# Performance work log

Hardware: AMD Instinct MI355X
Metric: run time of the kernel (lower is better)

Reference implementation:

```python
import jax, jax.numpy as jnp
import numpy as np

B, C, H, W = 2, 256, 128, 128
NUM_CLASSES = 80
HIDDEN = 4
STRIDE = 8
NMS_CAND = 1000
IOU_THR = 0.65
MAX_DET = 100
PRIOR_BIAS = float(-np.log((1.0 - 0.01) / 0.01))  # RetinaNet-style prior prob bias


def _conv1x1(x, w, b):
    # x: [B,C,H,W], w: [O,C], b: [O]
    return jnp.einsum('bchw,oc->bohw', x, w) + b[None, :, None, None]


def _head(x, w_in, b_in, w_hid, b_hid, w_out, b_out):
    # ProjConv in-layer -> residual ProjConv hidden layers (kernel_size=1, skip=True) -> ProjConv out-layer
    x = _conv1x1(x, w_in, b_in)
    def step(h, wb):
        w, b = wb
        return h + _conv1x1(h, w, b), None
    x, _ = jax.lax.scan(step, x, (w_hid, b_hid))
    return _conv1x1(x, w_out, b_out)


def _nms_keep(boxes):
    # boxes: [K,4] in xyxy, pre-sorted by descending score
    x1, y1, x2, y2 = boxes[:, 0], boxes[:, 1], boxes[:, 2], boxes[:, 3]
    area = jnp.clip(x2 - x1, 0) * jnp.clip(y2 - y1, 0)
    lt = jnp.maximum(boxes[:, None, :2], boxes[None, :, :2])
    rb = jnp.minimum(boxes[:, None, 2:], boxes[None, :, 2:])
    wh = jnp.clip(rb - lt, 0)
    inter = wh[..., 0] * wh[..., 1]
    iou = inter / (area[:, None] + area[None, :] - inter + 1e-6)
    idx = jnp.arange(NMS_CAND)
    def body(i, keep):
        sup = (iou[i] > IOU_THR) & (idx > i) & keep[i]
        return keep & ~sup
    return jax.lax.fori_loop(0, NMS_CAND, body, jnp.ones((NMS_CAND,), bool))


def setup_inputs() -> dict:
    key = jax.random.key(0)
    ks = jax.random.split(key, 10)
    s = 0.02
    d = {'feat': jax.random.normal(ks[0], (B, C, H, W), jnp.float32)}
    d['cls_w_in'] = s * jax.random.normal(ks[1], (C, C), jnp.float32)
    d['cls_b_in'] = jnp.zeros((C,), jnp.float32)
    d['cls_w_hid'] = s * jax.random.normal(ks[2], (HIDDEN, C, C), jnp.float32)
    d['cls_b_hid'] = jnp.zeros((HIDDEN, C), jnp.float32)
    d['cls_w_out'] = s * jax.random.normal(ks[3], (NUM_CLASSES + 1, C), jnp.float32)
    d['cls_b_out'] = jnp.full((NUM_CLASSES + 1,), PRIOR_BIAS, jnp.float32)
    d['obj_w_in'] = s * jax.random.normal(ks[4], (C, C), jnp.float32)
    d['obj_b_in'] = jnp.zeros((C,), jnp.float32)
    d['obj_w_hid'] = s * jax.random.normal(ks[5], (HIDDEN, C, C), jnp.float32)
    d['obj_b_hid'] = jnp.zeros((HIDDEN, C), jnp.float32)
    d['obj_w_out'] = s * jax.random.normal(ks[6], (2, C), jnp.float32)
    d['obj_b_out'] = jnp.full((2,), PRIOR_BIAS, jnp.float32)
    d['box_w_in'] = s * jax.random.normal(ks[7], (C, C), jnp.float32)
    d['box_b_in'] = jnp.zeros((C,), jnp.float32)
    d['box_w_hid'] = s * jax.random.normal(ks[8], (HIDDEN, C, C), jnp.float32)
    d['box_b_hid'] = jnp.zeros((HIDDEN, C), jnp.float32)
    d['box_w_out'] = s * jax.random.normal(ks[9], (4, C), jnp.float32)
    d['box_b_out'] = jnp.zeros((4,), jnp.float32)
    return d


def reference(feat, cls_w_in, cls_b_in, cls_w_hid, cls_b_hid, cls_w_out, cls_b_out,
              obj_w_in, obj_b_in, obj_w_hid, obj_b_hid, obj_w_out, obj_b_out,
              box_w_in, box_b_in, box_w_hid, box_b_hid, box_w_out, box_b_out):
    cls_logits = _head(feat, cls_w_in, cls_b_in, cls_w_hid, cls_b_hid, cls_w_out, cls_b_out)
    obj_logits = _head(feat, obj_w_in, obj_b_in, obj_w_hid, obj_b_hid, obj_w_out, obj_b_out)
    box_logits = _head(feat, box_w_in, box_b_in, box_w_hid, box_b_hid, box_w_out, box_b_out)

    # per-location scores: class prob (excluding background channel) * objectness prob
    cls_prob = jax.nn.sigmoid(cls_logits[:, :NUM_CLASSES])        # [B,80,H,W]
    obj_prob = jax.nn.sigmoid(obj_logits[:, :1])                  # [B,1,H,W]
    sc = cls_prob * obj_prob
    score = sc.max(axis=1).reshape(B, -1)                         # [B,HW]
    label = sc.argmax(axis=1).reshape(B, -1)                      # [B,HW]

    # FCOS-style decode of (l,t,r,b) deltas around grid points
    xs = (jnp.arange(W, dtype=feat.dtype) + 0.5) * STRIDE
    ys = (jnp.arange(H, dtype=feat.dtype) + 0.5) * STRIDE
    px = jnp.broadcast_to(xs[None, :], (H, W)).reshape(-1)
    py = jnp.broadcast_to(ys[:, None], (H, W)).reshape(-1)
    ltrb = jnp.exp(box_logits).reshape(B, 4, -1) * STRIDE         # [B,4,HW]
    boxes = jnp.stack([px[None] - ltrb[:, 0], py[None] - ltrb[:, 1],
                       px[None] + ltrb[:, 2], py[None] + ltrb[:, 3]], axis=-1)  # [B,HW,4]

    # candidate selection + NMS + final top detections
    cand_sc, idx = jax.lax.top_k(score, NMS_CAND)                 # sorted descending
    cand_box = jnp.take_along_axis(boxes, idx[:, :, None], axis=1)
    cand_lab = jnp.take_along_axis(label, idx, axis=1)
    keep = jax.vmap(_nms_keep)(cand_box)                          # [B,K] bool
    det_sc, fin_idx = jax.lax.top_k(cand_sc * keep, MAX_DET)
    det_box = jnp.take_along_axis(cand_box, fin_idx[:, :, None], axis=1)
    det_lab = jnp.take_along_axis(cand_lab, fin_idx, axis=1)
    return det_box, det_sc, det_lab
```

## Files before the change

### kernel.cpp

```cpp
#include <hip/hip_runtime.h>
#include <math.h>

typedef unsigned int u32;
typedef unsigned long long u64;

#define HWSZ 16384
#define NCAND 1000
#define CAP 1024
#define NDET 100

__device__ __forceinline__ float sigmoidf_(float x) {
  return 1.0f / (1.0f + expf(-x));
}

__device__ __forceinline__ void wave_stagger(int wid) {
  switch (wid) {
    case 1: __builtin_amdgcn_s_sleep(1); break;
    case 2: __builtin_amdgcn_s_sleep(2); break;
    case 3: __builtin_amdgcn_s_sleep(3); break;
    case 4: __builtin_amdgcn_s_sleep(4); break;
    case 5: __builtin_amdgcn_s_sleep(5); break;
    case 6: __builtin_amdgcn_s_sleep(6); break;
    case 7: __builtin_amdgcn_s_sleep(7); break;
    case 8: __builtin_amdgcn_s_sleep(8); break;
    case 9: __builtin_amdgcn_s_sleep(9); break;
    case 10: __builtin_amdgcn_s_sleep(10); break;
    case 11: __builtin_amdgcn_s_sleep(11); break;
    case 12: __builtin_amdgcn_s_sleep(12); break;
    case 13: __builtin_amdgcn_s_sleep(13); break;
    case 14: __builtin_amdgcn_s_sleep(14); break;
    case 15: __builtin_amdgcn_s_sleep(15); break;
    default: break;
  }
}

template <int NROWS, bool FULLROWS>
__device__ __forceinline__ void run_gemm(const float* __restrict__ Wm,
                                         const float (*X)[128], int rbase,
                                         int p0, float2 acc[16]) {
#pragma unroll
  for (int r = 0; r < 16; ++r) {
    acc[r].x = 0.f;
    acc[r].y = 0.f;
  }
  wave_stagger(rbase >> 4);
  if (rbase < NROWS) {
    for (int kb = 0; kb < 64; ++kb) {
      float2 xv0 = *(const float2*)&X[kb * 4 + 0][p0];
      float2 xv1 = *(const float2*)&X[kb * 4 + 1][p0];
      float2 xv2 = *(const float2*)&X[kb * 4 + 2][p0];
      float2 xv3 = *(const float2*)&X[kb * 4 + 3][p0];
#pragma unroll
      for (int r = 0; r < 16; ++r) {
        if (FULLROWS || rbase + r < NROWS) {
          const float4 wv =
              *(const float4*)(Wm + (size_t)(rbase + r) * 256 + kb * 4);
          acc[r].x += wv.x * xv0.x;
          acc[r].y += wv.x * xv0.y;
          acc[r].x += wv.y * xv1.x;
          acc[r].y += wv.y * xv1.y;
          acc[r].x += wv.z * xv2.x;
          acc[r].y += wv.z * xv2.y;
          acc[r].x += wv.w * xv3.x;
          acc[r].y += wv.w * xv3.y;
        }
      }
    }
  }
}

__global__ __launch_bounds__(1024, 4) void heads_fused(
    const float* __restrict__ feat, const float* __restrict__ ow_in,
    const float* __restrict__ ob_in, const float* __restrict__ ow_hid,
    const float* __restrict__ ob_hid, const float* __restrict__ ow_out,
    const float* __restrict__ ob_out, const float* __restrict__ cw_in,
    const float* __restrict__ cb_in, const float* __restrict__ cw_hid,
    const float* __restrict__ cb_hid, const float* __restrict__ cw_out,
    const float* __restrict__ cb_out, float* __restrict__ score,
    int* __restrict__ label) {
  __shared__ __align__(16) float X[256][128];
  __shared__ float objL[128];
  __shared__ float smax[5][128];
  __shared__ int sarg[5][128];

  const int tid = threadIdx.x;
  const int wid = __builtin_amdgcn_readfirstlane(tid >> 6);
  const int ln = tid & 63;
  const int p0 = 2 * ln;
  const int rbase = wid * 16;
  const int batch = blockIdx.x >> 7;
  const int pbase = (blockIdx.x & 127) * 128;
  const float* fb = feat + (size_t)batch * 256 * HWSZ;

  for (int head = 0; head < 2; ++head) {
    const float* w_in = head ? cw_in : ow_in;
    const float* b_in = head ? cb_in : ob_in;
    const float* w_hid = head ? cw_hid : ow_hid;
    const float* b_hid = head ? cb_hid : ob_hid;

#pragma unroll
    for (int m = 0; m < 8; ++m) {
      int f4 = tid + 1024 * m;
      int c = f4 >> 5, col4 = (f4 & 31) * 4;
      *(float4*)&X[c][col4] =
          *(const float4*)(fb + (size_t)c * HWSZ + pbase + col4);
    }
    __syncthreads();

    float2 acc[16];
    for (int s = 0; s < 5; ++s) {
      const float* Wm = (s == 0) ? w_in : (w_hid + (size_t)(s - 1) * 65536);
      const float* bs = (s == 0) ? b_in : (b_hid + (s - 1) * 256);
      run_gemm<256, true>(Wm, X, rbase, p0, acc);
      __syncthreads();
#pragma unroll
      for (int r = 0; r < 16; ++r) {
        float b = bs[rbase + r];
        float2 v = make_float2(acc[r].x + b, acc[r].y + b);
        if (s > 0) {
          v.x += X[rbase + r][p0];
          v.y += X[rbase + r][p0 + 1];
        }
        *(float2*)&X[rbase + r][p0] = v;
      }
      __syncthreads();
    }

    if (head == 0) {
      run_gemm<2, false>(ow_out, X, rbase, p0, acc);
      if (wid == 0) {
        float bo = ob_out[0];
        objL[p0] = sigmoidf_(acc[0].x + bo);
        objL[p0 + 1] = sigmoidf_(acc[0].y + bo);
      }
      __syncthreads();
    } else {
      run_gemm<80, true>(cw_out, X, rbase, p0, acc);
      if (rbase < 80) {
        float ob0 = objL[p0], ob1 = objL[p0 + 1];
        float best0 = -1.f, best1 = -1.f;
        int a0 = 0, a1 = 0;
#pragma unroll
        for (int r = 0; r < 16; ++r) {
          float bb = cb_out[rbase + r];
          float s0 = sigmoidf_(acc[r].x + bb) * ob0;
          float s1 = sigmoidf_(acc[r].y + bb) * ob1;
          if (s0 > best0) {
            best0 = s0;
            a0 = rbase + r;
          }
          if (s1 > best1) {
            best1 = s1;
            a1 = rbase + r;
          }
        }
        smax[wid][p0] = best0;
        sarg[wid][p0] = a0;
        smax[wid][p0 + 1] = best1;
        sarg[wid][p0 + 1] = a1;
      }
      __syncthreads();
      if (tid < 128) {
        float best = -1.f;
        int ba = 0;
        for (int g = 0; g < 5; ++g) {
          float m = smax[g][tid];
          if (m > best) {
            best = m;
            ba = sarg[g][tid];
          }
        }
        score[batch * HWSZ + pbase + tid] = best;
        label[batch * HWSZ + pbase + tid] = ba;
      }
    }
  }
}

__global__ __launch_bounds__(1024) void box_all(
    const float* __restrict__ feat, const int* __restrict__ cand_idx,
    const float* __restrict__ w_in, const float* __restrict__ b_in,
    const float* __restrict__ w_hid, const float* __restrict__ b_hid,
    const float* __restrict__ w_out, const float* __restrict__ b_out,
    float* __restrict__ cand_box) {
  __shared__ float h[256][8];
  const int tid = threadIdx.x;
  const int batch = blockIdx.x >> 7;
  const int cbase = (blockIdx.x & 127) * 8;
  const float* fb = feat + (size_t)batch * 256 * HWSZ;

  for (int i = tid; i < 2048; i += 1024) {
    int k = i >> 3, c = i & 7;
    int r = cbase + c;
    float v = 0.f;
    if (r < NCAND) {
      int hw = cand_idx[batch * CAP + r];
      v = fb[(size_t)k * HWSZ + hw];
    }
    h[k][c] = v;
  }
  __syncthreads();

  const int wid = tid >> 6, ln = tid & 63;
  const int c = ln & 7, rr = ln >> 3;
  const int r0 = wid * 16 + rr, r1 = wid * 16 + 8 + rr;

  for (int s = 0; s < 5; ++s) {
    const float* Wm = (s == 0) ? w_in : (w_hid + (size_t)(s - 1) * 65536);
    const float* bs = (s == 0) ? b_in : (b_hid + (s - 1) * 256);
    float a0 = 0.f, a1 = 0.f;
    for (int kb = 0; kb < 64; ++kb) {
      float4 w0 = *(const float4*)&Wm[(size_t)r0 * 256 + kb * 4];
      float4 w1 = *(const float4*)&Wm[(size_t)r1 * 256 + kb * 4];
      float x0 = h[kb * 4 + 0][c], x1 = h[kb * 4 + 1][c];
      float x2 = h[kb * 4 + 2][c], x3 = h[kb * 4 + 3][c];
      a0 += w0.x * x0;
      a0 += w0.y * x1;
      a0 += w0.z * x2;
      a0 += w0.w * x3;
      a1 += w1.x * x0;
      a1 += w1.y * x1;
      a1 += w1.z * x2;
      a1 += w1.w * x3;
    }
    __syncthreads();
    float v0 = a0 + bs[r0], v1 = a1 + bs[r1];
    if (s > 0) {
      v0 += h[r0][c];
      v1 += h[r1][c];
    }
    h[r0][c] = v0;
    h[r1][c] = v1;
    __syncthreads();
  }

  if (tid < 32) {
    int row = tid >> 3, cc = tid & 7;
    int r = cbase + cc;
    if (r < NCAND) {
      float s = 0.f;
      for (int k = 0; k < 256; ++k) s += w_out[row * 256 + k] * h[k][cc];
      s += b_out[row];
      float e = expf(s) * 8.f;
      int hw = cand_idx[batch * CAP + r];
      int hh = hw >> 7, wwp = hw & 127;
      float px = (wwp + 0.5f) * 8.f, py = (hh + 0.5f) * 8.f;
      float coord = (row == 0)   ? px - e
                    : (row == 1) ? py - e
                    : (row == 2) ? px + e
                                 : py + e;
      cand_box[(size_t)(batch * CAP + r) * 4 + row] = coord;
    }
  }
}

__device__ __forceinline__ void suffix2048(u32* hist, int tid) {
  for (int d = 1; d < 2048; d <<= 1) {
    u32 v0 = hist[tid] + ((tid + d < 2048) ? hist[tid + d] : 0u);
    u32 v1 =
        hist[tid + 1024] + ((tid + 1024 + d < 2048) ? hist[tid + 1024 + d] : 0u);
    __syncthreads();
    hist[tid] = v0;
    hist[tid + 1024] = v1;
    __syncthreads();
  }
}

__global__ __launch_bounds__(1024) void topk_kernel(
    const float* __restrict__ score, const int* __restrict__ label,
    float* __restrict__ cand_sc, int* __restrict__ cand_idx,
    int* __restrict__ cand_lab) {
  __shared__ u32 hist[2048];
  __shared__ u64 buf[CAP];
  __shared__ u32 tiebuf[2048];
  __shared__ int sres[2];
  __shared__ int cA, cT;
  const int tid = threadIdx.x;
  const int b = blockIdx.x;
  const int base = b * HWSZ;
  u32 bits[16];
#pragma unroll
  for (int m = 0; m < 16; ++m)
    bits[m] = __float_as_uint(score[base + tid + 1024 * m]);

  int K = NCAND;
  u32 hi = 0;
  u32 thresh = 0;
  for (int lev = 0; lev < 3; ++lev) {
    hist[tid] = 0;
    hist[tid + 1024] = 0;
    __syncthreads();
#pragma unroll
    for (int m = 0; m < 16; ++m) {
      u32 v = bits[m];
      bool ok;
      int bin;
      if (lev == 0) {
        ok = true;
        bin = v >> 21;
      } else if (lev == 1) {
        ok = ((v >> 21) == hi);
        bin = (v >> 10) & 2047;
      } else {
        ok = ((v >> 10) == hi);
        bin = v & 1023;
      }
      if (ok) atomicAdd(&hist[bin], 1u);
    }
    __syncthreads();
    suffix2048(hist, tid);
#pragma unroll
    for (int e = 0; e < 2; ++e) {
      int i = tid + e * 1024;
      int Si = (int)hist[i];
      int Sn = (i + 1 < 2048) ? (int)hist[i + 1] : 0;
      if (Si >= K && Sn < K) {
        sres[0] = i;
        sres[1] = Sn;
      }
    }
    __syncthreads();
    int B = sres[0];
    K -= sres[1];
    if (lev == 0) hi = (u32)B;
    else if (lev == 1) hi = (hi << 11) | (u32)B;
    else thresh = (hi << 10) | (u32)B;
    __syncthreads();
  }
  const int T = K;

  if (tid == 0) {
    cA = 0;
    cT = 0;
  }
  __syncthreads();
#pragma unroll
  for (int m = 0; m < 16; ++m) {
    u32 v = bits[m];
    int idxp = tid + 1024 * m;
    if (v > thresh) {
      int pos = atomicAdd(&cA, 1);
      buf[pos] = ((u64)(~v) << 32) | (u32)idxp;
    } else if (v == thresh) {
      int pos = atomicAdd(&cT, 1);
      if (pos < 2048) tiebuf[pos] = (u32)idxp;
    }
  }
  __syncthreads();
  const int A = cA;
  int nT = cT < 2048 ? cT : 2048;
  for (int i = tid; i < 2048; i += 1024)
    if (i >= nT) tiebuf[i] = 0xFFFFFFFFu;
  __syncthreads();
  if (nT > 1) {
    for (int k = 2; k <= 2048; k <<= 1)
      for (int j = k >> 1; j > 0; j >>= 1) {
#pragma unroll
        for (int e = 0; e < 2; ++e) {
          int i = tid + e * 1024;
          int l = i ^ j;
          if (l > i) {
            u32 a = tiebuf[i], bb = tiebuf[l];
            bool up = ((i & k) == 0);
            if ((a > bb) == up) {
              tiebuf[i] = bb;
              tiebuf[l] = a;
            }
          }
        }
        __syncthreads();
      }
  }
  for (int t2 = tid; t2 < T; t2 += 1024)
    buf[A + t2] = ((u64)(~thresh) << 32) | tiebuf[t2];
  for (int i = tid; i < CAP; i += 1024)
    if (i >= NCAND) buf[i] = 0xFFFFFFFFFFFFFFFFull;
  __syncthreads();
  for (int k = 2; k <= 1024; k <<= 1)
    for (int j = k >> 1; j > 0; j >>= 1) {
      int i = tid, l = i ^ j;
      if (l > i) {
        u64 a = buf[i], bb = buf[l];
        bool up = ((i & k) == 0);
        if ((a > bb) == up) {
          buf[i] = bb;
          buf[l] = a;
        }
      }
      __syncthreads();
    }
  if (tid < NCAND) {
    u64 kv = buf[tid];
    u32 sb = ~(u32)(kv >> 32);
    int pix = (int)(kv & 0xFFFFFFFFull);
    cand_sc[b * CAP + tid] = __uint_as_float(sb);
    cand_idx[b * CAP + tid] = pix;
    cand_lab[b * CAP + tid] = label[base + pix];
  }
}

__global__ __launch_bounds__(1024) void nms_mask(
    const float* __restrict__ cand_box, u64* __restrict__ mask) {
  int bid = blockIdx.x;
  int b = bid / NCAND, i = bid % NCAND;
  int j = threadIdx.x;
  const float* bi = cand_box + (size_t)(b * CAP + i) * 4;
  float ix1 = bi[0], iy1 = bi[1], ix2 = bi[2], iy2 = bi[3];
  bool pred = false;
  if (j < NCAND && j > i) {
    const float* bj = cand_box + (size_t)(b * CAP + j) * 4;
    float jx1 = bj[0], jy1 = bj[1], jx2 = bj[2], jy2 = bj[3];
    float ai = fmaxf(ix2 - ix1, 0.f) * fmaxf(iy2 - iy1, 0.f);
    float aj = fmaxf(jx2 - jx1, 0.f) * fmaxf(jy2 - jy1, 0.f);
    float lx = fmaxf(ix1, jx1), ly = fmaxf(iy1, jy1);
    float rx = fminf(ix2, jx2), ry = fminf(iy2, jy2);
    float w = fmaxf(rx - lx, 0.f), h = fmaxf(ry - ly, 0.f);
    float inter = w * h;
    float iou = inter / (ai + aj - inter + 1e-6f);
    pred = iou > 0.65f;
  }
  u64 word = __ballot(pred);
  if ((j & 63) == 0) mask[(size_t)b * 16384 + i * 16 + (j >> 6)] = word;
}

__global__ void nms_finish(const u64* __restrict__ mask,
                           const float* __restrict__ cand_sc,
                           const int* __restrict__ cand_lab,
                           const float* __restrict__ cand_box,
                           float* __restrict__ out) {
  __shared__ u64 M[16000];
  int b = blockIdx.x, lane = threadIdx.x;
  for (int m = lane; m < 16000; m += 64) M[m] = mask[(size_t)b * 16384 + m];
  __syncthreads();
  u64 kw = 0ull;
  if (lane < 15) kw = ~0ull;
  else if (lane == 15) kw = (1ull << 40) - 1;
  for (int i = 0; i < NCAND; ++i) {
    u64 wi = __shfl(kw, i >> 6);
    if ((wi >> (i & 63)) & 1ull) {
      if (lane < 16) kw &= ~M[i * 16 + lane];
    }
  }
  u64 valid = 0ull;
  if (lane < 15) valid = ~0ull;
  else if (lane == 15) valid = (1ull << 40) - 1;
  kw &= valid;
  u64 sup = valid & ~kw;
  int ck = __popcll(kw), cs = __popcll(sup);
  int preK = 0, preS = 0, totK = 0;
  for (int q = 0; q < 16; ++q) {
    int vk = __shfl(ck, q), vs = __shfl(cs, q);
    if (q < lane) {
      preK += vk;
      preS += vs;
    }
    totK += vk;
  }
  float* obox = out;
  float* osc = out + 2 * NDET * 4;
  float* olab = out + 2 * NDET * 4 + 2 * NDET;
  if (lane < 16) {
    u64 m = kw;
    int pos = preK;
    while (m) {
      int bit = __ffsll((unsigned long long)m) - 1;
      m &= m - 1;
      int j = lane * 64 + bit;
      if (pos < NDET) {
        osc[b * NDET + pos] = cand_sc[b * CAP + j];
        olab[b * NDET + pos] = (float)cand_lab[b * CAP + j];
        const float* bx = cand_box + (size_t)(b * CAP + j) * 4;
        float* dst = obox + (size_t)(b * NDET + pos) * 4;
        dst[0] = bx[0];
        dst[1] = bx[1];
        dst[2] = bx[2];
        dst[3] = bx[3];
      }
      ++pos;
    }
    m = sup;
    pos = totK + preS;
    while (m) {
      int bit = __ffsll((unsigned long long)m) - 1;
      m &= m - 1;
      int j = lane * 64 + bit;
      if (pos < NDET) {
        osc[b * NDET + pos] = 0.0f;
        olab[b * NDET + pos] = (float)cand_lab[b * CAP + j];
        const float* bx = cand_box + (size_t)(b * CAP + j) * 4;
        float* dst = obox + (size_t)(b * NDET + pos) * 4;
        dst[0] = bx[0];
        dst[1] = bx[1];
        dst[2] = bx[2];
        dst[3] = bx[3];
      }
      ++pos;
    }
  }
}

extern "C" void kernel_launch(void* const* d_in, const int* in_sizes, int n_in,
                              void* d_out, int out_size, void* d_ws,
                              size_t ws_size, hipStream_t stream) {
  (void)in_sizes;
  (void)n_in;
  (void)out_size;
  (void)ws_size;
  const float* feat = (const float*)d_in[0];
  const float* cls_w_in = (const float*)d_in[1];
  const float* cls_b_in = (const float*)d_in[2];
  const float* cls_w_hid = (const float*)d_in[3];
  const float* cls_b_hid = (const float*)d_in[4];
  const float* cls_w_out = (const float*)d_in[5];
  const float* cls_b_out = (const float*)d_in[6];
  const float* obj_w_in = (const float*)d_in[7];
  const float* obj_b_in = (const float*)d_in[8];
  const float* obj_w_hid = (const float*)d_in[9];
  const float* obj_b_hid = (const float*)d_in[10];
  const float* obj_w_out = (const float*)d_in[11];
  const float* obj_b_out = (const float*)d_in[12];
  const float* box_w_in = (const float*)d_in[13];
  const float* box_b_in = (const float*)d_in[14];
  const float* box_w_hid = (const float*)d_in[15];
  const float* box_b_hid = (const float*)d_in[16];
  const float* box_w_out = (const float*)d_in[17];
  const float* box_b_out = (const float*)d_in[18];
  float* out = (float*)d_out;

  char* w = (char*)d_ws;
  float* scoreArr = (float*)w;
  int* labelArr = (int*)(w + 131072);
  float* cand_sc = (float*)(w + 262144);
  int* cand_idx = (int*)(w + 270336);
  int* cand_lab = (int*)(w + 278528);
  float* cand_box = (float*)(w + 286720);
  u64* maskArr = (u64*)(w + 319488);

  heads_fused<<<256, 1024, 0, stream>>>(
      feat, obj_w_in, obj_b_in, obj_w_hid, obj_b_hid, obj_w_out, obj_b_out,
      cls_w_in, cls_b_in, cls_w_hid, cls_b_hid, cls_w_out, cls_b_out, scoreArr,
      labelArr);
  topk_kernel<<<2, 1024, 0, stream>>>(scoreArr, labelArr, cand_sc, cand_idx,
                                      cand_lab);
  box_all<<<256, 1024, 0, stream>>>(feat, cand_idx, box_w_in, box_b_in,
                                    box_w_hid, box_b_hid, box_w_out, box_b_out,
                                    cand_box);
  nms_mask<<<2000, 1024, 0, stream>>>(cand_box, maskArr);
  nms_finish<<<2, 64, 0, stream>>>(maskArr, cand_sc, cand_lab, cand_box, out);
}
```

Measured before the change: 783.3 us.

## Stage conv weights through double-buffered LDS instead of per-wave global loads

New measurement: 943.7 us. 1.2x slower.

```diff
diff --git a/kernel.cpp b/kernel.cpp
--- a/kernel.cpp
+++ b/kernel.cpp
@@ -13,59 +13,64 @@
   return 1.0f / (1.0f + expf(-x));
 }
 
-__device__ __forceinline__ void wave_stagger(int wid) {
-  switch (wid) {
-    case 1: __builtin_amdgcn_s_sleep(1); break;
-    case 2: __builtin_amdgcn_s_sleep(2); break;
-    case 3: __builtin_amdgcn_s_sleep(3); break;
-    case 4: __builtin_amdgcn_s_sleep(4); break;
-    case 5: __builtin_amdgcn_s_sleep(5); break;
-    case 6: __builtin_amdgcn_s_sleep(6); break;
-    case 7: __builtin_amdgcn_s_sleep(7); break;
-    case 8: __builtin_amdgcn_s_sleep(8); break;
-    case 9: __builtin_amdgcn_s_sleep(9); break;
-    case 10: __builtin_amdgcn_s_sleep(10); break;
-    case 11: __builtin_amdgcn_s_sleep(11); break;
-    case 12: __builtin_amdgcn_s_sleep(12); break;
-    case 13: __builtin_amdgcn_s_sleep(13); break;
-    case 14: __builtin_amdgcn_s_sleep(14); break;
-    case 15: __builtin_amdgcn_s_sleep(15); break;
-    default: break;
-  }
-}
-
 template <int NROWS, bool FULLROWS>
-__device__ __forceinline__ void run_gemm(const float* __restrict__ Wm,
-                                         const float (*X)[128], int rbase,
+__device__ __forceinline__ void gemm_lds(const float* __restrict__ Wm,
+                                         const float (*X)[128],
+                                         float (*Wb)[2048], int tid, int rbase,
                                          int p0, float2 acc[16]) {
 #pragma unroll
   for (int r = 0; r < 16; ++r) {
     acc[r].x = 0.f;
     acc[r].y = 0.f;
   }
-  wave_stagger(rbase >> 4);
-  if (rbase < NROWS) {
-    for (int kb = 0; kb < 64; ++kb) {
-      float2 xv0 = *(const float2*)&X[kb * 4 + 0][p0];
-      float2 xv1 = *(const float2*)&X[kb * 4 + 1][p0];
-      float2 xv2 = *(const float2*)&X[kb * 4 + 2][p0];
-      float2 xv3 = *(const float2*)&X[kb * 4 + 3][p0];
+  const int strow = tid >> 2;
+  const int stk = (tid & 3) * 2;
+  const bool stage_on = (tid < NROWS * 4);
+  const bool compute_on = (rbase < NROWS);
+
+  if (stage_on) {
+    float2 pv = *(const float2*)(Wm + (size_t)strow * 256 + stk);
+    *(float2*)&Wb[0][strow * 8 + stk] = pv;
+  }
+  __syncthreads();
+
+  for (int w = 0; w < 32; ++w) {
+    const int buf = w & 1;
+    float2 nv;
+    const bool pre = stage_on && (w + 1 < 32);
+    if (pre) nv = *(const float2*)(Wm + (size_t)strow * 256 + (w + 1) * 8 + stk);
+
+    if (compute_on) {
+      float2 xv[8];
+#pragma unroll
+      for (int j = 0; j < 8; ++j)
+        xv[j] = *(const float2*)&X[w * 8 + j][p0];
 #pragma unroll
       for (int r = 0; r < 16; ++r) {
         if (FULLROWS || rbase + r < NROWS) {
-          const float4 wv =
-              *(const float4*)(Wm + (size_t)(rbase + r) * 256 + kb * 4);
-          acc[r].x += wv.x * xv0.x;
-          acc[r].y += wv.x * xv0.y;
-          acc[r].x += wv.y * xv1.x;
-          acc[r].y += wv.y * xv1.y;
-          acc[r].x += wv.z * xv2.x;
-          acc[r].y += wv.z * xv2.y;
-          acc[r].x += wv.w * xv3.x;
-          acc[r].y += wv.w * xv3.y;
+          const float4 wa = *(const float4*)&Wb[buf][(rbase + r) * 8];
+          const float4 wb2 = *(const float4*)&Wb[buf][(rbase + r) * 8 + 4];
+          acc[r].x += wa.x * xv[0].x;
+          acc[r].y += wa.x * xv[0].y;
+          acc[r].x += wa.y * xv[1].x;
+          acc[r].y += wa.y * xv[1].y;
+          acc[r].x += wa.z * xv[2].x;
+          acc[r].y += wa.z * xv[2].y;
+          acc[r].x += wa.w * xv[3].x;
+          acc[r].y += wa.w * xv[3].y;
+          acc[r].x += wb2.x * xv[4].x;
+          acc[r].y += wb2.x * xv[4].y;
+          acc[r].x += wb2.y * xv[5].x;
+          acc[r].y += wb2.y * xv[5].y;
+          acc[r].x += wb2.z * xv[6].x;
+          acc[r].y += wb2.z * xv[6].y;
+          acc[r].x += wb2.w * xv[7].x;
+          acc[r].y += wb2.w * xv[7].y;
         }
       }
     }
+    if (pre) *(float2*)&Wb[buf ^ 1][strow * 8 + stk] = nv;
+    __syncthreads();
   }
 }
 
@@ -79,6 +84,7 @@
     const float* __restrict__ cb_out, float* __restrict__ score,
     int* __restrict__ label) {
   __shared__ __align__(16) float X[256][128];
+  __shared__ __align__(16) float Wb[2][2048];
   __shared__ float objL[128];
   __shared__ float smax[5][128];
   __shared__ int sarg[5][128];
@@ -111,8 +117,7 @@
     for (int s = 0; s < 5; ++s) {
       const float* Wm = (s == 0) ? w_in : (w_hid + (size_t)(s - 1) * 65536);
       const float* bs = (s == 0) ? b_in : (b_hid + (s - 1) * 256);
-      run_gemm<256, true>(Wm, X, rbase, p0, acc);
-      __syncthreads();
+      gemm_lds<256, true>(Wm, X, Wb, tid, rbase, p0, acc);
 #pragma unroll
       for (int r = 0; r < 16; ++r) {
         float b = bs[rbase + r];
@@ -123,11 +128,10 @@
         }
         *(float2*)&X[rbase + r][p0] = v;
       }
-      __syncthreads();
     }
 
     if (head == 0) {
-      run_gemm<2, false>(ow_out, X, rbase, p0, acc);
+      gemm_lds<2, false>(ow_out, X, Wb, tid, rbase, p0, acc);
       if (wid == 0) {
         float bo = ob_out[0];
         objL[p0] = sigmoidf_(acc[0].x + bo);
@@ -135,7 +139,7 @@
       }
       __syncthreads();
     } else {
-      run_gemm<80, true>(cw_out, X, rbase, p0, acc);
+      gemm_lds<80, true>(cw_out, X, Wb, tid, rbase, p0, acc);
       if (rbase < 80) {
         float ob0 = objL[p0], ob1 = objL[p0 + 1];
         float best0 = -1.f, best1 = -1.f;
```

## Stage weight tiles through double-buffered LDS instead of per-wave global loads

Applied to the files above, without the earlier changes.

After: 926.5 us. +18.3%, slower.

```diff
diff --git a/kernel.cpp b/kernel.cpp
--- a/kernel.cpp
+++ b/kernel.cpp
@@ -13,63 +13,66 @@
   return 1.0f / (1.0f + expf(-x));
 }
 
-__device__ __forceinline__ void wave_stagger(int wid) {
-  switch (wid) {
-    case 1: __builtin_amdgcn_s_sleep(1); break;
-    case 2: __builtin_amdgcn_s_sleep(2); break;
-    case 3: __builtin_amdgcn_s_sleep(3); break;
-    case 4: __builtin_amdgcn_s_sleep(4); break;
-    case 5: __builtin_amdgcn_s_sleep(5); break;
-    case 6: __builtin_amdgcn_s_sleep(6); break;
-    case 7: __builtin_amdgcn_s_sleep(7); break;
-    case 8: __builtin_amdgcn_s_sleep(8); break;
-    case 9: __builtin_amdgcn_s_sleep(9); break;
-    case 10: __builtin_amdgcn_s_sleep(10); break;
-    case 11: __builtin_amdgcn_s_sleep(11); break;
-    case 12: __builtin_amdgcn_s_sleep(12); break;
-    case 13: __builtin_amdgcn_s_sleep(13); break;
-    case 14: __builtin_amdgcn_s_sleep(14); break;
-    case 15: __builtin_amdgcn_s_sleep(15); break;
-    default: break;
-  }
-}
-
 template <int NROWS, bool FULLROWS>
 __device__ __forceinline__ void run_gemm(const float* __restrict__ Wm,
-                                         const float (*X)[128], int rbase,
+                                         const float (*X)[128],
+                                         float (*Wb)[2048], int tid, int rbase,
                                          int p0, float2 acc[16]) {
 #pragma unroll
   for (int r = 0; r < 16; ++r) {
     acc[r].x = 0.f;
     acc[r].y = 0.f;
   }
-  wave_stagger(rbase >> 4);
-  if (rbase < NROWS) {
-    for (int kb = 0; kb < 64; ++kb) {
-      float2 xv0 = *(const float2*)&X[kb * 4 + 0][p0];
-      float2 xv1 = *(const float2*)&X[kb * 4 + 1][p0];
-      float2 xv2 = *(const float2*)&X[kb * 4 + 2][p0];
-      float2 xv3 = *(const float2*)&X[kb * 4 + 3][p0];
-#pragma unroll
-      for (int r = 0; r < 16; ++r) {
-        if (FULLROWS || rbase + r < NROWS) {
-          const float4 wv =
-              *(const float4*)(Wm + (size_t)(rbase + r) * 256 + kb * 4);
-          acc[r].x += wv.x * xv0.x;
-          acc[r].y += wv.x * xv0.y;
-          acc[r].x += wv.y * xv1.x;
-          acc[r].y += wv.y * xv1.y;
-          acc[r].x += wv.z * xv2.x;
-          acc[r].y += wv.z * xv2.y;
-          acc[r].x += wv.w * xv3.x;
-          acc[r].y += wv.w * xv3.y;
+  const int srow = tid >> 2;
+  const int sq = (tid & 3) * 2;
+  const bool sg = srow < NROWS;
+  const bool cg = rbase < NROWS;
+
+  if (sg) {
+    float2 v = *(const float2*)(Wm + (size_t)srow * 256 + sq);
+    *(float2*)&Wb[0][srow * 8 + sq] = v;
+  }
+  __syncthreads();
+
+#pragma unroll 1
+  for (int wn = 0; wn < 32; ++wn) {
+    const int buf = wn & 1;
+    float2 nv;
+    const bool pre = sg && (wn + 1 < 32);
+    if (pre)
+      nv = *(const float2*)(Wm + (size_t)srow * 256 + (wn + 1) * 8 + sq);
+
+    if (cg) {
+#pragma unroll
+      for (int j = 0; j < 2; ++j) {
+        const int kb = wn * 2 + j;
+        const float2 xv0 = *(const float2*)&X[kb * 4 + 0][p0];
+        const float2 xv1 = *(const float2*)&X[kb * 4 + 1][p0];
+        const float2 xv2 = *(const float2*)&X[kb * 4 + 2][p0];
+        const float2 xv3 = *(const float2*)&X[kb * 4 + 3][p0];
+#pragma unroll
+        for (int r = 0; r < 16; ++r) {
+          if (FULLROWS || rbase + r < NROWS) {
+            const float4 wv =
+                *(const float4*)&Wb[buf][(rbase + r) * 8 + j * 4];
+            acc[r].x += wv.x * xv0.x;
+            acc[r].y += wv.x * xv0.y;
+            acc[r].x += wv.y * xv1.x;
+            acc[r].y += wv.y * xv1.y;
+            acc[r].x += wv.z * xv2.x;
+            acc[r].y += wv.z * xv2.y;
+            acc[r].x += wv.w * xv3.x;
+            acc[r].y += wv.w * xv3.y;
+          }
         }
       }
     }
-  }
-}
-
-__global__ __launch_bounds__(1024, 4) void heads_fused(
+    if (pre) *(float2*)&Wb[buf ^ 1][srow * 8 + sq] = nv;
+    __syncthreads();
+  }
+}
+
+__global__ __launch_bounds__(1024) void heads_fused(
     const float* __restrict__ feat, const float* __restrict__ ow_in,
     const float* __restrict__ ob_in, const float* __restrict__ ow_hid,
     const float* __restrict__ ob_hid, const float* __restrict__ ow_out,
@@ -79,6 +82,7 @@
     const float* __restrict__ cb_out, float* __restrict__ score,
     int* __restrict__ label) {
   __shared__ __align__(16) float X[256][128];
+  __shared__ __align__(16) float Wb[2][2048];
   __shared__ float objL[128];
   __shared__ float smax[5][128];
   __shared__ int sarg[5][128];
@@ -111,8 +115,7 @@
     for (int s = 0; s < 5; ++s) {
       const float* Wm = (s == 0) ? w_in : (w_hid + (size_t)(s - 1) * 65536);
       const float* bs = (s == 0) ? b_in : (b_hid + (s - 1) * 256);
-      run_gemm<256, true>(Wm, X, rbase, p0, acc);
-      __syncthreads();
+      run_gemm<256, true>(Wm, X, Wb, tid, rbase, p0, acc);
 #pragma unroll
       for (int r = 0; r < 16; ++r) {
         float b = bs[rbase + r];
@@ -127,7 +130,7 @@
     }
 
     if (head == 0) {
-      run_gemm<2, false>(ow_out, X, rbase, p0, acc);
+      run_gemm<2, false>(ow_out, X, Wb, tid, rbase, p0, acc);
       if (wid == 0) {
         float bo = ob_out[0];
         objL[p0] = sigmoidf_(acc[0].x + bo);
@@ -135,7 +138,7 @@
       }
       __syncthreads();
     } else {
-      run_gemm<80, true>(cw_out, X, rbase, p0, acc);
+      run_gemm<80, true>(cw_out, X, Wb, tid, rbase, p0, acc);
       if (rbase < 80) {
         float ob0 = objL[p0], ob1 = objL[p0 + 1];
         float best0 = -1.f, best1 = -1.f;
```
